# Optimization experiments

Measured on AMD Instinct MI355X. Metric: run time of the kernel, lower is better.

## Reference

```python
import jax, jax.numpy as jnp
import numpy as np

GRID_SIZE = 5
SPLINE_ORDER = 3
KK = 3  # kernel side
N_CONVS = 4
GRID_LO, GRID_HI = -1.0, 1.0


def b_splines(x, grid, k):
    # x: (N, in_features), grid: (grid_size + 2k + 1,) shared across in_features
    # returns (N, in_features, grid_size + k)
    x = x[..., None]
    bases = ((x >= grid[:-1]) & (x < grid[1:])).astype(x.dtype)
    for p in range(1, k + 1):
        left = (x - grid[:-(p + 1)]) / (grid[p:-1] - grid[:-(p + 1)])
        right = (grid[p + 1:] - x) / (grid[p + 1:] - grid[1:-p])
        bases = left * bases[..., :-1] + right * bases[..., 1:]
    return bases


def setup_inputs() -> dict:
    key = jax.random.key(0)
    k1, k2, k3, k4 = jax.random.split(key, 4)
    in_f = KK * KK
    x = jax.random.normal(k1, (8, 16, 96, 96), dtype=jnp.float32)
    # per-conv KANLinear params (out_features = 1), stacked over n_convs
    base_w = jax.random.normal(k2, (N_CONVS, in_f), dtype=jnp.float32) * (1.0 / np.sqrt(in_f))
    spline_w = jax.random.normal(k3, (N_CONVS, in_f, GRID_SIZE + SPLINE_ORDER), dtype=jnp.float32) * 0.1
    spline_scaler = jax.random.normal(k4, (N_CONVS, in_f), dtype=jnp.float32) * (1.0 / np.sqrt(in_f))
    h = (GRID_HI - GRID_LO) / GRID_SIZE
    grid = jnp.arange(-SPLINE_ORDER, GRID_SIZE + SPLINE_ORDER + 1, dtype=jnp.float32) * h + GRID_LO
    return {"x": x, "base_w": base_w, "spline_w": spline_w,
            "spline_scaler": spline_scaler, "grid": grid}


def reference(x, base_w, spline_w, spline_scaler, grid):
    B, C, H, W = x.shape
    # unfold (im2col): (B, C*KK*KK, Ho, Wo), feature dim ordered channel-slowest like torch Unfold
    patches = jax.lax.conv_general_dilated_patches(x, (KK, KK), (1, 1), 'VALID')
    Ho, Wo = patches.shape[2], patches.shape[3]
    # (B, C, Ho, Wo, KK*KK) -> flat rows (N, in_features)
    p = patches.reshape(B, C, KK * KK, Ho, Wo).transpose(0, 1, 3, 4, 2).reshape(-1, KK * KK)
    bases = b_splines(p, grid, SPLINE_ORDER)              # (N, in, G+k)
    sw = spline_w * spline_scaler[..., None]              # scaled spline weight (c, in, G+k)
    out = (jnp.einsum('ni,ci->nc', jax.nn.silu(p), base_w)
           + jnp.einsum('nig,cig->nc', bases, sw))        # (N, n_convs)
    # output channel index = kern + channel * n_convs
    out = out.reshape(B, C, Ho, Wo, N_CONVS).transpose(0, 1, 4, 2, 3)
    return out.reshape(B, C * N_CONVS, Ho, Wo)
```

## Files before the change

### kernel.cpp

```cpp
#include <hip/hip_runtime.h>
#include <math.h>

constexpr int Bb = 8, Cc = 16, Hh = 96, Ww = 96;
constexpr int Ho = 94, Wo = 94;
constexpr int NC = 4;
constexpr int PLANE = Ho * Wo;

constexpr int TX = 16, TYS = 47;
constexpr int IX = 18, IY = 49;
constexpr int NXT = 6, NYT = 2;
constexpr int FS = 12;
constexpr int ROWU = IX * FS;
constexpr int ROWB = ROWU * 2;
constexpr int BWS = 72;

typedef __attribute__((ext_vector_type(4))) float f32x4;
typedef __attribute__((ext_vector_type(8))) short bf16x8;

template <int N> struct IC { static constexpr int value = N; };

__device__ __forceinline__ unsigned short f2bf(float f) {
    union { float f; unsigned u; } a; a.f = f;
    unsigned r = a.u + 0x7fffu + ((a.u >> 16) & 1u);
    return (unsigned short)(r >> 16);
}
__device__ __forceinline__ unsigned pk2(float a, float b) {
    return (unsigned)f2bf(a) | ((unsigned)f2bf(b) << 16);
}
__device__ __forceinline__ bf16x8 mkfrag(unsigned a0, unsigned a1, unsigned a2, unsigned a3) {
    union { unsigned u[4]; bf16x8 v; } t;
    t.u[0] = a0; t.u[1] = a1; t.u[2] = a2; t.u[3] = a3;
    return t.v;
}
__device__ __forceinline__ float dpp_shr4(float v) {
    return __int_as_float(__builtin_amdgcn_update_dpp(0, __float_as_int(v), 0x114, 0xF, 0xF, true));
}
__device__ __forceinline__ float dpp_shr8(float v) {
    return __int_as_float(__builtin_amdgcn_update_dpp(0, __float_as_int(v), 0x118, 0xF, 0xF, true));
}

struct F4 { float v0, v1, v2, v3; } __attribute__((packed, aligned(4)));

__global__ __launch_bounds__(256, 6)
void kan_conv_kernel(const float* __restrict__ x,
                     const float* __restrict__ base_w,
                     const float* __restrict__ spline_w,
                     const float* __restrict__ spline_scaler,
                     const float* __restrict__ grid,
                     float* __restrict__ out)
{
    __shared__ unsigned short feat[IY * ROWU + 256];
    __shared__ unsigned short Bw[16 * BWS];

    const int tid = threadIdx.x;
    int blk = blockIdx.x;
    const int xt = blk % NXT; blk /= NXT;
    const int yt = blk % NYT; blk /= NYT;
    const int c  = blk % Cc;
    const int b  = blk / Cc;
    const int ox0 = xt * TX;
    const int oy0 = yt * TYS;

    {
        const int col = tid >> 4;
        const int k0  = (tid & 15) * 4;
        const int d = col >> 2, cv = col & 3;
        unsigned short w[4];
#pragma unroll
        for (int e = 0; e < 4; ++e) {
            const int k = k0 + e;
            float val = 0.f;
            if (col < 12 && k < 36) {
                const int j = k / 12, o = k - 12 * j;
                const int wi = cv * 9 + 3 * d + j;
                if (o < 8)       val = spline_scaler[wi] * spline_w[wi * 8 + o];
                else if (o == 8) val = base_w[wi];
            }
            w[e] = f2bf(val);
        }
        *reinterpret_cast<uint2*>(&Bw[col * BWS + k0]) =
            make_uint2((unsigned)w[0] | ((unsigned)w[1] << 16),
                       (unsigned)w[2] | ((unsigned)w[3] << 16));
        feat[IY * ROWU + tid] = 0;
    }

    const float g0   = grid[0];
    const float invh = 1.0f / (grid[1] - g0);
    const float* xplane = x + (size_t)(b * Cc + c) * Hh * Ww;

    for (int p = tid; p < IX * IY; p += 256) {
        const int py = p / IX, px = p % IX;
        const int gy = oy0 + py;
        const int gx = ox0 + px;
        const float v = (gx < Ww) ? xplane[gy * Ww + gx] : 0.0f;

        const float sl = v / (1.0f + __expf(-v));

        const float u = (v - g0) * invh;
        int j = (int)u;
        if (!(u >= 0.0f && u < 11.0f)) j = -100;
        const float t  = u - (float)j;
        const float t2 = t * t, t3 = t2 * t;
        const float omt = 1.0f - t;
        const float B0 = (1.0f / 6.0f) * omt * omt * omt;
        const float B1 = (1.0f / 6.0f) * (3.0f * t3 - 6.0f * t2 + 4.0f);
        const float B2 = (1.0f / 6.0f) * (-3.0f * t3 + 3.0f * t2 + 3.0f * t + 1.0f);
        const float B3 = (1.0f / 6.0f) * t3;

        float bb[8];
#pragma unroll
        for (int k = 0; k < 8; ++k) {
            float r = 0.0f;
            r = (j == k + 3) ? B0 : r;
            r = (j == k + 2) ? B1 : r;
            r = (j == k + 1) ? B2 : r;
            r = (j == k    ) ? B3 : r;
            bb[k] = r;
        }

        unsigned short* fp = &feat[p * FS];
        *reinterpret_cast<uint2*>(fp + 0) = make_uint2(pk2(bb[0], bb[1]), pk2(bb[2], bb[3]));
        *reinterpret_cast<uint2*>(fp + 4) = make_uint2(pk2(bb[4], bb[5]), pk2(bb[6], bb[7]));
        *reinterpret_cast<uint2*>(fp + 8) = make_uint2(pk2(sl, 0.0f), 0u);
    }

    __syncthreads();

    const int lane = tid & 63;
    const int wv   = tid >> 6;
    const int r    = lane & 15;
    const int g    = lane >> 4;

    const bf16x8 wb1 = *reinterpret_cast<const bf16x8*>(&Bw[r * BWS +  0 + 8 * g]);
    const bf16x8 wb2 = *reinterpret_cast<const bf16x8*>(&Bw[r * BWS + 32 + 8 * g]);

    const char* fb = (const char*)feat + (12 * wv) * ROWB + 24 * r + 16 * g;

    const int cvl = r & 3;
    float* obase = out + ((size_t)((b * Cc + c) * NC) + cvl) * PLANE;
    const bool storer = (r >= 8) && (r < 12);
    const int oxs = ox0 + 4 * g;
    const bool fullstore = (oxs + 3 < Wo);

    f32x4 sA, sB, sC;
    const f32x4 zz = {0.f, 0.f, 0.f, 0.f};
    sA = zz; sB = zz; sC = zz;

    auto kstep = [&](auto ITC, f32x4& cur, f32x4& p1, f32x4& p2) {
        constexpr int IT = decltype(ITC)::value;
        const uint2 lo = *reinterpret_cast<const uint2*>(fb + IT * ROWB);
        const uint2 hi = *reinterpret_cast<const uint2*>(fb + IT * ROWB + 8);
        const uint2 x2 = *reinterpret_cast<const uint2*>(fb + IT * ROWB + 64);
        cur = __builtin_amdgcn_mfma_f32_16x16x32_bf16(mkfrag(lo.x, lo.y, hi.x, hi.y), wb1, zz, 0, 0, 0);
        cur = __builtin_amdgcn_mfma_f32_16x16x32_bf16(mkfrag(x2.x, x2.y, x2.x, x2.y), wb2, cur, 0, 0, 0);
        if constexpr (IT >= 2) {
            const int lrow = 12 * wv + IT - 2;
            if (lrow < TYS) {
                f32x4 tot;
                tot[0] = cur[0] + dpp_shr4(p1[0]) + dpp_shr8(p2[0]);
                tot[1] = cur[1] + dpp_shr4(p1[1]) + dpp_shr8(p2[1]);
                tot[2] = cur[2] + dpp_shr4(p1[2]) + dpp_shr8(p2[2]);
                tot[3] = cur[3] + dpp_shr4(p1[3]) + dpp_shr8(p2[3]);
                if (storer) {
                    const int oy = oy0 + lrow;
                    float* op = obase + oy * Wo + oxs;
                    if (fullstore) {
                        F4 s; s.v0 = tot[0]; s.v1 = tot[1]; s.v2 = tot[2]; s.v3 = tot[3];
                        *reinterpret_cast<F4*>(op) = s;
                    } else {
#pragma unroll
                        for (int e = 0; e < 4; ++e)
                            if (oxs + e < Wo) op[e] = tot[e];
                    }
                }
            }
        }
    };

    kstep(IC<0>{},  sA, sC, sB);
    kstep(IC<1>{},  sB, sA, sC);
    kstep(IC<2>{},  sC, sB, sA);
    kstep(IC<3>{},  sA, sC, sB);
    kstep(IC<4>{},  sB, sA, sC);
    kstep(IC<5>{},  sC, sB, sA);
    kstep(IC<6>{},  sA, sC, sB);
    kstep(IC<7>{},  sB, sA, sC);
    kstep(IC<8>{},  sC, sB, sA);
    kstep(IC<9>{},  sA, sC, sB);
    kstep(IC<10>{}, sB, sA, sC);
    kstep(IC<11>{}, sC, sB, sA);
    kstep(IC<12>{}, sA, sC, sB);
    kstep(IC<13>{}, sB, sA, sC);
}

extern "C" void kernel_launch(void* const* d_in, const int* in_sizes, int n_in,
                              void* d_out, int out_size, void* d_ws, size_t ws_size,
                              hipStream_t stream) {
    const float* x             = (const float*)d_in[0];
    const float* base_w        = (const float*)d_in[1];
    const float* spline_w      = (const float*)d_in[2];
    const float* spline_scaler = (const float*)d_in[3];
    const float* grid          = (const float*)d_in[4];
    float* out = (float*)d_out;

    const int nblocks = Bb * Cc * NXT * NYT;
    kan_conv_kernel<<<nblocks, 256, 0, stream>>>(x, base_w, spline_w,
                                                 spline_scaler, grid, out);
}
```

Baseline: 20.04 us.

## Split feature precompute into separate kernel writing bf16 features to workspace

Moves the per-pixel B-spline and SiLU feature computation into a separate kernel that writes packed bf16 feature records to global workspace. The conv kernel then reads those records directly from global memory instead of staging them in shared memory, with a different row-chunk tiling (4 chunks of 24 rows, 6 rows per wave). This removes the halo recomputation and the LDS staging, but adds a second launch and a large global write plus reread (24 bytes per pixel versus 4 for the input), which may dominate at this size.

```diff
diff --git a/kernel.cpp b/kernel.cpp
--- a/kernel.cpp
+++ b/kernel.cpp
@@ -5,14 +5,17 @@
 constexpr int Ho = 94, Wo = 94;
 constexpr int NC = 4;
 constexpr int PLANE = Ho * Wo;
-
-constexpr int TX = 16, TYS = 47;
-constexpr int IX = 18, IY = 49;
-constexpr int NXT = 6, NYT = 2;
-constexpr int FS = 12;
-constexpr int ROWU = IX * FS;
-constexpr int ROWB = ROWU * 2;
-constexpr int BWS = 72;
+constexpr int NPLANES = Bb * Cc;
+constexpr int PPX = Hh * Ww;
+
+constexpr int FS   = 12;
+constexpr int RECB = FS * 2;
+constexpr int ROWB = Ww * RECB;
+constexpr size_t PLB = (size_t)PPX * RECB;
+constexpr int BWS  = 72;
+
+constexpr int NXT = 6;
+constexpr int NYC = 4;
 
 typedef __attribute__((ext_vector_type(4))) float f32x4;
 typedef __attribute__((ext_vector_type(8))) short bf16x8;
@@ -41,25 +44,63 @@
 
 struct F4 { float v0, v1, v2, v3; } __attribute__((packed, aligned(4)));
 
-__global__ __launch_bounds__(256, 6)
-void kan_conv_kernel(const float* __restrict__ x,
+__global__ __launch_bounds__(256)
+void kan_feat_kernel(const float* __restrict__ x,
+                     const float* __restrict__ grid,
+                     unsigned short* __restrict__ ws)
+{
+    const int idx = blockIdx.x * 256 + threadIdx.x;
+    const float g0   = grid[0];
+    const float invh = 1.0f / (grid[1] - g0);
+
+    const float v = x[idx];
+
+    const float sl = v / (1.0f + __expf(-v));
+
+    const float u = (v - g0) * invh;
+    int j = (int)u;
+    if (!(u >= 0.0f && u < 11.0f)) j = -100;
+    const float t  = u - (float)j;
+    const float t2 = t * t, t3 = t2 * t;
+    const float omt = 1.0f - t;
+    const float B0 = (1.0f / 6.0f) * omt * omt * omt;
+    const float B1 = (1.0f / 6.0f) * (3.0f * t3 - 6.0f * t2 + 4.0f);
+    const float B2 = (1.0f / 6.0f) * (-3.0f * t3 + 3.0f * t2 + 3.0f * t + 1.0f);
+    const float B3 = (1.0f / 6.0f) * t3;
+
+    float bb[8];
+#pragma unroll
+    for (int k = 0; k < 8; ++k) {
+        float r = 0.0f;
+        r = (j == k + 3) ? B0 : r;
+        r = (j == k + 2) ? B1 : r;
+        r = (j == k + 1) ? B2 : r;
+        r = (j == k    ) ? B3 : r;
+        bb[k] = r;
+    }
+
+    unsigned short* fp = ws + (size_t)idx * FS;
+    *reinterpret_cast<uint2*>(fp + 0) = make_uint2(pk2(bb[0], bb[1]), pk2(bb[2], bb[3]));
+    *reinterpret_cast<uint2*>(fp + 4) = make_uint2(pk2(bb[4], bb[5]), pk2(bb[6], bb[7]));
+    *reinterpret_cast<uint2*>(fp + 8) = make_uint2(pk2(sl, 0.0f), 0u);
+}
+
+__global__ __launch_bounds__(256)
+void kan_conv_kernel(const unsigned short* __restrict__ ws,
                      const float* __restrict__ base_w,
                      const float* __restrict__ spline_w,
                      const float* __restrict__ spline_scaler,
-                     const float* __restrict__ grid,
                      float* __restrict__ out)
 {
-    __shared__ unsigned short feat[IY * ROWU + 256];
     __shared__ unsigned short Bw[16 * BWS];
 
     const int tid = threadIdx.x;
     int blk = blockIdx.x;
-    const int xt = blk % NXT; blk /= NXT;
-    const int yt = blk % NYT; blk /= NYT;
-    const int c  = blk % Cc;
-    const int b  = blk / Cc;
-    const int ox0 = xt * TX;
-    const int oy0 = yt * TYS;
+    const int xt    = blk % NXT; blk /= NXT;
+    const int chunk = blk % NYC; blk /= NYC;
+    const int plane = blk;
+    const int ox0 = xt * 16;
+    const int c0  = chunk * 24;
 
     {
         const int col = tid >> 4;
@@ -81,49 +122,7 @@
         *reinterpret_cast<uint2*>(&Bw[col * BWS + k0]) =
             make_uint2((unsigned)w[0] | ((unsigned)w[1] << 16),
                        (unsigned)w[2] | ((unsigned)w[3] << 16));
-        feat[IY * ROWU + tid] = 0;
     }
-
-    const float g0   = grid[0];
-    const float invh = 1.0f / (grid[1] - g0);
-    const float* xplane = x + (size_t)(b * Cc + c) * Hh * Ww;
-
-    for (int p = tid; p < IX * IY; p += 256) {
-        const int py = p / IX, px = p % IX;
-        const int gy = oy0 + py;
-        const int gx = ox0 + px;
-        const float v = (gx < Ww) ? xplane[gy * Ww + gx] : 0.0f;
-
-        const float sl = v / (1.0f + __expf(-v));
-
-        const float u = (v - g0) * invh;
-        int j = (int)u;
-        if (!(u >= 0.0f && u < 11.0f)) j = -100;
-        const float t  = u - (float)j;
-        const float t2 = t * t, t3 = t2 * t;
-        const float omt = 1.0f - t;
-        const float B0 = (1.0f / 6.0f) * omt * omt * omt;
-        const float B1 = (1.0f / 6.0f) * (3.0f * t3 - 6.0f * t2 + 4.0f);
-        const float B2 = (1.0f / 6.0f) * (-3.0f * t3 + 3.0f * t2 + 3.0f * t + 1.0f);
-        const float B3 = (1.0f / 6.0f) * t3;
-
-        float bb[8];
-#pragma unroll
-        for (int k = 0; k < 8; ++k) {
-            float r = 0.0f;
-            r = (j == k + 3) ? B0 : r;
-            r = (j == k + 2) ? B1 : r;
-            r = (j == k + 1) ? B2 : r;
-            r = (j == k    ) ? B3 : r;
-            bb[k] = r;
-        }
-
-        unsigned short* fp = &feat[p * FS];
-        *reinterpret_cast<uint2*>(fp + 0) = make_uint2(pk2(bb[0], bb[1]), pk2(bb[2], bb[3]));
-        *reinterpret_cast<uint2*>(fp + 4) = make_uint2(pk2(bb[4], bb[5]), pk2(bb[6], bb[7]));
-        *reinterpret_cast<uint2*>(fp + 8) = make_uint2(pk2(sl, 0.0f), 0u);
-    }
-
     __syncthreads();
 
     const int lane = tid & 63;
@@ -134,10 +133,15 @@
     const bf16x8 wb1 = *reinterpret_cast<const bf16x8*>(&Bw[r * BWS +  0 + 8 * g]);
     const bf16x8 wb2 = *reinterpret_cast<const bf16x8*>(&Bw[r * BWS + 32 + 8 * g]);
 
-    const char* fb = (const char*)feat + (12 * wv) * ROWB + 24 * r + 16 * g;
+    const int ry = c0 + 6 * wv;
+
+    const int colb = ((ox0 + r < 93) ? (ox0 + r) : 93) * RECB;
+    const char* pbase  = (const char*)ws + plane * PLB + colb;
+    const char* base   = pbase + 16 * g;
+    const char* basex  = pbase + ((g == 0) ? 64 : 0);
 
     const int cvl = r & 3;
-    float* obase = out + ((size_t)((b * Cc + c) * NC) + cvl) * PLANE;
+    float* obase = out + ((size_t)(plane * NC) + cvl) * PLANE;
     const bool storer = (r >= 8) && (r < 12);
     const int oxs = ox0 + 4 * g;
     const bool fullstore = (oxs + 3 < Wo);
@@ -148,21 +152,22 @@
 
     auto kstep = [&](auto ITC, f32x4& cur, f32x4& p1, f32x4& p2) {
         constexpr int IT = decltype(ITC)::value;
-        const uint2 lo = *reinterpret_cast<const uint2*>(fb + IT * ROWB);
-        const uint2 hi = *reinterpret_cast<const uint2*>(fb + IT * ROWB + 8);
-        const uint2 x2 = *reinterpret_cast<const uint2*>(fb + IT * ROWB + 64);
+        const int rr = (ry + IT <= 95) ? (ry + IT) : 95;
+        const size_t ro = (size_t)rr * ROWB;
+        const uint2 lo = *reinterpret_cast<const uint2*>(base + ro);
+        const uint2 hi = *reinterpret_cast<const uint2*>(base + ro + 8);
+        const uint2 x2 = *reinterpret_cast<const uint2*>(basex + ro);
         cur = __builtin_amdgcn_mfma_f32_16x16x32_bf16(mkfrag(lo.x, lo.y, hi.x, hi.y), wb1, zz, 0, 0, 0);
         cur = __builtin_amdgcn_mfma_f32_16x16x32_bf16(mkfrag(x2.x, x2.y, x2.x, x2.y), wb2, cur, 0, 0, 0);
         if constexpr (IT >= 2) {
-            const int lrow = 12 * wv + IT - 2;
-            if (lrow < TYS) {
+            const int oy = ry + IT - 2;
+            if (oy < Ho) {
                 f32x4 tot;
                 tot[0] = cur[0] + dpp_shr4(p1[0]) + dpp_shr8(p2[0]);
                 tot[1] = cur[1] + dpp_shr4(p1[1]) + dpp_shr8(p2[1]);
                 tot[2] = cur[2] + dpp_shr4(p1[2]) + dpp_shr8(p2[2]);
                 tot[3] = cur[3] + dpp_shr4(p1[3]) + dpp_shr8(p2[3]);
                 if (storer) {
-                    const int oy = oy0 + lrow;
                     float* op = obase + oy * Wo + oxs;
                     if (fullstore) {
                         F4 s; s.v0 = tot[0]; s.v1 = tot[1]; s.v2 = tot[2]; s.v3 = tot[3];
@@ -177,20 +182,14 @@
         }
     };
 
-    kstep(IC<0>{},  sA, sC, sB);
-    kstep(IC<1>{},  sB, sA, sC);
-    kstep(IC<2>{},  sC, sB, sA);
-    kstep(IC<3>{},  sA, sC, sB);
-    kstep(IC<4>{},  sB, sA, sC);
-    kstep(IC<5>{},  sC, sB, sA);
-    kstep(IC<6>{},  sA, sC, sB);
-    kstep(IC<7>{},  sB, sA, sC);
-    kstep(IC<8>{},  sC, sB, sA);
-    kstep(IC<9>{},  sA, sC, sB);
-    kstep(IC<10>{}, sB, sA, sC);
-    kstep(IC<11>{}, sC, sB, sA);
-    kstep(IC<12>{}, sA, sC, sB);
-    kstep(IC<13>{}, sB, sA, sC);
+    kstep(IC<0>{}, sA, sC, sB);
+    kstep(IC<1>{}, sB, sA, sC);
+    kstep(IC<2>{}, sC, sB, sA);
+    kstep(IC<3>{}, sA, sC, sB);
+    kstep(IC<4>{}, sB, sA, sC);
+    kstep(IC<5>{}, sC, sB, sA);
+    kstep(IC<6>{}, sA, sC, sB);
+    kstep(IC<7>{}, sB, sA, sC);
 }
 
 extern "C" void kernel_launch(void* const* d_in, const int* in_sizes, int n_in,
@@ -202,8 +201,12 @@
     const float* spline_scaler = (const float*)d_in[3];
     const float* grid          = (const float*)d_in[4];
     float* out = (float*)d_out;
-
-    const int nblocks = Bb * Cc * NXT * NYT;
-    kan_conv_kernel<<<nblocks, 256, 0, stream>>>(x, base_w, spline_w,
-                                                 spline_scaler, grid, out);
-}
+    unsigned short* feat_ws = (unsigned short*)d_ws;
+
+    const int ablocks = (NPLANES * PPX) / 256;
+    kan_feat_kernel<<<ablocks, 256, 0, stream>>>(x, grid, feat_ws);
+
+    const int bblocks = NPLANES * NYC * NXT;
+    kan_conv_kernel<<<bblocks, 256, 0, stream>>>(feat_ws, base_w, spline_w,
+                                                 spline_scaler, out);
+}
```

Measured after the change: 33.49 us. 67.1% more time.
